# Performance work log

Hardware: AMD Instinct MI355X
Metric: run time of the kernel (lower is better)

The kernel has to match this reference:

```python
import jax, jax.numpy as jnp
import numpy as np

E, K = 8, 2            # num_experts, top_k
H, F = 1024, 1024      # hidden_size, ffn_hidden_size
T = 2048               # tokens (batch*seq)


def setup_inputs() -> dict:
    key = jax.random.key(0)
    k1, k2, k3, k4 = jax.random.split(key, 4)
    x = jax.random.normal(k1, (T, H), jnp.float32)
    gate_w = jax.random.normal(k2, (E, H), jnp.float32) * 0.02   # router FastLinear weight [E, H]
    w1_v1 = jax.random.normal(k3, (E, 2 * F, H), jnp.float32) * 0.02  # cat([w1, v1], dim=0) per expert
    w2 = jax.random.normal(k4, (E, H, F), jnp.float32) * 0.02    # down-proj FastLinear weight [H, F]
    return {"x": x, "gate_w": gate_w, "w1_v1": w1_v1, "w2": w2}


def reference(x, gate_w, w1_v1, w2):
    # Router: logits -> softmax -> top-k gating weights (DBRX style)
    logits = x @ gate_w.T                       # [T, E]
    probs = jax.nn.softmax(logits, axis=-1)
    top_w, top_e = jax.lax.top_k(probs, K)      # [T, K]
    # Dense combine matrix [T, E]: gating weight if expert selected, else 0
    combine = jnp.zeros((x.shape[0], E), x.dtype).at[
        jnp.arange(x.shape[0])[:, None], top_e
    ].add(top_w)
    # Per-expert GLU MLP, batched over experts (grouped GEMM equivalent)
    gv = jnp.einsum('th,efh->etf', x, w1_v1)    # [E, T, 2F]
    g, v = jnp.split(gv, 2, axis=-1)            # each [E, T, F]
    hidden = jax.nn.silu(g) * v                 # [E, T, F]
    outs = jnp.einsum('etf,ehf->eth', hidden, w2)  # [E, T, H]
    # Combine: weighted sum over selected experts
    return jnp.einsum('eth,te->th', outs, combine)  # [T, H]
```

## Files before the change

kernel.cpp:

```cpp
#include <hip/hip_runtime.h>
#include <hip/hip_bf16.h>

#define T_TOK 2048
#define HID   1024
#define FF    1024
#define NE    8
#define CNT_STRIDE 64
#define RTOK 16

using short8   = __attribute__((ext_vector_type(8))) short;
using ushort8v = __attribute__((ext_vector_type(8))) unsigned short;
using f32x4    = __attribute__((ext_vector_type(4))) float;

__device__ __forceinline__ unsigned short f32_to_bf16(float f) {
  union { float f; unsigned int u; } v; v.f = f;
  unsigned int r = v.u + 0x7fffu + ((v.u >> 16) & 1u);
  return (unsigned short)(r >> 16);
}

__global__ __launch_bounds__(256) void convert_kernel(const float* __restrict__ src,
                                                      unsigned short* __restrict__ dst,
                                                      int n4) {
  int i = blockIdx.x * 256 + threadIdx.x;
  if (i >= n4) return;
  const float4 v = ((const float4*)src)[i];
  ushort4 o;
  o.x = f32_to_bf16(v.x); o.y = f32_to_bf16(v.y);
  o.z = f32_to_bf16(v.z); o.w = f32_to_bf16(v.w);
  ((ushort4*)dst)[i] = o;
}

__global__ __launch_bounds__(256) void router_kernel(const float* __restrict__ x,
                                                     const float* __restrict__ gw,
                                                     int* __restrict__ counts,
                                                     int* __restrict__ toks,
                                                     float* __restrict__ wts) {
  __shared__ float gws[NE * HID];
  __shared__ int   s_e[RTOK * 2];
  __shared__ float s_w[RTOK * 2];
  int tid = threadIdx.x;
  int lane = tid & 63, wid = tid >> 6;
  int t0 = blockIdx.x * RTOK;

  float4 greg[8];
#pragma unroll
  for (int j = 0; j < 8; ++j) greg[j] = ((const float4*)gw)[j * 256 + tid];

  float4 xv[4][4];
#pragma unroll
  for (int tk = 0; tk < 4; ++tk) {
    const float4* xr4 = (const float4*)(x + (size_t)(t0 + wid * 4 + tk) * HID);
#pragma unroll
    for (int c = 0; c < 4; ++c) xv[tk][c] = xr4[c * 64 + lane];
  }

#pragma unroll
  for (int j = 0; j < 8; ++j) ((float4*)&gws[0])[j * 256 + tid] = greg[j];
  __syncthreads();

  float acc[4][NE];
#pragma unroll
  for (int tk = 0; tk < 4; ++tk)
#pragma unroll
    for (int e = 0; e < NE; ++e) acc[tk][e] = 0.f;

#pragma unroll
  for (int c = 0; c < 4; ++c) {
#pragma unroll
    for (int e = 0; e < NE; ++e) {
      const float4 gv = *(const float4*)&gws[e * HID + (c * 64 + lane) * 4];
#pragma unroll
      for (int tk = 0; tk < 4; ++tk) {
        acc[tk][e] = fmaf(xv[tk][c].x, gv.x, acc[tk][e]);
        acc[tk][e] = fmaf(xv[tk][c].y, gv.y, acc[tk][e]);
        acc[tk][e] = fmaf(xv[tk][c].z, gv.z, acc[tk][e]);
        acc[tk][e] = fmaf(xv[tk][c].w, gv.w, acc[tk][e]);
      }
    }
  }

#pragma unroll
  for (int tk = 0; tk < 4; ++tk) {
#pragma unroll
    for (int off = 32; off >= 1; off >>= 1) {
#pragma unroll
      for (int e = 0; e < NE; ++e) acc[tk][e] += __shfl_xor(acc[tk][e], off);
    }
    if (lane == 0) {
      int local = wid * 4 + tk;
      float m = acc[tk][0];
#pragma unroll
      for (int e = 1; e < NE; ++e) m = fmaxf(m, acc[tk][e]);
      float p[NE], s = 0.f;
#pragma unroll
      for (int e = 0; e < NE; ++e) { p[e] = __expf(acc[tk][e] - m); s += p[e]; }
      float inv = 1.f / s;

      int e1 = 0; float b1 = p[0];
#pragma unroll
      for (int e = 1; e < NE; ++e) if (p[e] > b1) { b1 = p[e]; e1 = e; }
      int e2 = -1; float b2 = -1.f;
#pragma unroll
      for (int e = 0; e < NE; ++e) if (e != e1 && p[e] > b2) { b2 = p[e]; e2 = e; }

      s_e[local * 2]     = e1;  s_w[local * 2]     = b1 * inv;
      s_e[local * 2 + 1] = e2;  s_w[local * 2 + 1] = b2 * inv;
    }
  }
  __syncthreads();

  if (tid < NE) {
    int c = 0;
#pragma unroll
    for (int i = 0; i < RTOK * 2; ++i) c += (s_e[i] == tid);
    if (c > 0) {
      int base = atomicAdd(&counts[tid * CNT_STRIDE], c);
      int p = 0;
      for (int i = 0; i < RTOK * 2; ++i) {
        if (s_e[i] == tid) {
          toks[tid * T_TOK + base + p] = t0 + (i >> 1);
          wts[tid * T_TOK + base + p] = s_w[i];
          ++p;
        }
      }
    }
  }
}

__global__ __launch_bounds__(256) void gemm1_kernel(const unsigned short* __restrict__ xb,
                                                    const unsigned short* __restrict__ w1b,
                                                    const int* __restrict__ counts,
                                                    const int* __restrict__ toks,
                                                    unsigned short* __restrict__ hidden) {
  int e = blockIdx.z;
  int cnt = counts[e * CNT_STRIDE];
  int m0 = blockIdx.y * 128;
  if (m0 >= cnt) return;
  int n0 = blockIdx.x * 64;
  const unsigned short* W = w1b + (size_t)e * (2 * FF * HID);

  __shared__ unsigned short sA[128 * 64];
  __shared__ unsigned short sBg[64 * 64];
  __shared__ unsigned short sBv[64 * 64];

  int tid = threadIdx.x;
  int lane = tid & 63, wid = tid >> 6;

  const unsigned short* aptr[4]; int adst[4];
#pragma unroll
  for (int j = 0; j < 4; ++j) {
    int q = tid + 256 * j;
    int row = q >> 3, u = q & 7;
    int gr = m0 + row;
    int tok = (gr < cnt) ? toks[e * T_TOK + gr] : 0;
    int su = u ^ (row & 7);
    aptr[j] = xb + (size_t)tok * HID + su * 8;
    adst[j] = row * 64 + u * 8;
  }
  const unsigned short* bgptr[2]; const unsigned short* bvptr[2]; int bdst[2];
#pragma unroll
  for (int j = 0; j < 2; ++j) {
    int q = tid + 256 * j;
    int row = q >> 3, u = q & 7;
    int su = u ^ (row & 7);
    bgptr[j] = W + (size_t)(n0 + row) * HID + su * 8;
    bvptr[j] = W + (size_t)(FF + n0 + row) * HID + su * 8;
    bdst[j] = row * 64 + u * 8;
  }

  f32x4 accg[2][4], accv[2][4];
#pragma unroll
  for (int m = 0; m < 2; ++m)
#pragma unroll
    for (int n = 0; n < 4; ++n) {
      accg[m][n] = (f32x4){0.f, 0.f, 0.f, 0.f};
      accv[m][n] = (f32x4){0.f, 0.f, 0.f, 0.f};
    }

  for (int k0 = 0; k0 < HID; k0 += 64) {
#pragma unroll
    for (int j = 0; j < 4; ++j)
      *(ushort8v*)&sA[adst[j]] = *(const ushort8v*)(aptr[j] + k0);
#pragma unroll
    for (int j = 0; j < 2; ++j) {
      *(ushort8v*)&sBg[bdst[j]] = *(const ushort8v*)(bgptr[j] + k0);
      *(ushort8v*)&sBv[bdst[j]] = *(const ushort8v*)(bvptr[j] + k0);
    }
    __syncthreads();
#pragma unroll
    for (int kk = 0; kk < 2; ++kk) {
      short8 af[2], bgf[4], bvf[4];
#pragma unroll
      for (int m = 0; m < 2; ++m) {
        int row = wid * 32 + m * 16 + (lane & 15);
        int u = (kk * 4 + (lane >> 4)) ^ (row & 7);
        af[m] = *(const short8*)&sA[row * 64 + u * 8];
      }
#pragma unroll
      for (int n = 0; n < 4; ++n) {
        int row = n * 16 + (lane & 15);
        int u = (kk * 4 + (lane >> 4)) ^ (row & 7);
        bgf[n] = *(const short8*)&sBg[row * 64 + u * 8];
        bvf[n] = *(const short8*)&sBv[row * 64 + u * 8];
      }
#pragma unroll
      for (int m = 0; m < 2; ++m)
#pragma unroll
        for (int n = 0; n < 4; ++n) {
          accg[m][n] = __builtin_amdgcn_mfma_f32_16x16x32_bf16(af[m], bgf[n], accg[m][n], 0, 0, 0);
          accv[m][n] = __builtin_amdgcn_mfma_f32_16x16x32_bf16(af[m], bvf[n], accv[m][n], 0, 0, 0);
        }
    }
    __syncthreads();
  }

  unsigned short* Hseg = hidden + (size_t)e * T_TOK * FF;
#pragma unroll
  for (int m = 0; m < 2; ++m) {
#pragma unroll
    for (int j = 0; j < 4; ++j) {
      int row = wid * 32 + m * 16 + (lane >> 4) * 4 + j;
      int gr = m0 + row;
      if (gr < cnt) {
#pragma unroll
        for (int n = 0; n < 4; ++n) {
          int col = n0 + n * 16 + (lane & 15);
          float g = accg[m][n][j];
          float v = accv[m][n][j];
          float val = (g / (1.f + __expf(-g))) * v;
          Hseg[(size_t)gr * FF + col] = f32_to_bf16(val);
        }
      }
    }
  }
}

__global__ __launch_bounds__(256) void gemm2_kernel(const unsigned short* __restrict__ hidden,
                                                    const unsigned short* __restrict__ w2b,
                                                    const int* __restrict__ counts,
                                                    const int* __restrict__ toks,
                                                    const float* __restrict__ wts,
                                                    float* __restrict__ out) {
  int e = blockIdx.z;
  int cnt = counts[e * CNT_STRIDE];
  int m0 = blockIdx.y * 128;
  if (m0 >= cnt) return;
  int n0 = blockIdx.x * 64;
  const unsigned short* A = hidden + (size_t)e * T_TOK * FF;
  const unsigned short* W = w2b + (size_t)e * HID * FF;

  __shared__ unsigned short sA[128 * 64];
  __shared__ unsigned short sB[64 * 64];

  int tid = threadIdx.x;
  int lane = tid & 63, wid = tid >> 6;

  const unsigned short* aptr[4]; int adst[4];
#pragma unroll
  for (int j = 0; j < 4; ++j) {
    int q = tid + 256 * j;
    int row = q >> 3, u = q & 7;
    int su = u ^ (row & 7);
    aptr[j] = A + (size_t)(m0 + row) * FF + su * 8;
    adst[j] = row * 64 + u * 8;
  }
  const unsigned short* bptr[2]; int bdst[2];
#pragma unroll
  for (int j = 0; j < 2; ++j) {
    int q = tid + 256 * j;
    int row = q >> 3, u = q & 7;
    int su = u ^ (row & 7);
    bptr[j] = W + (size_t)(n0 + row) * FF + su * 8;
    bdst[j] = row * 64 + u * 8;
  }

  f32x4 acc[2][4];
#pragma unroll
  for (int m = 0; m < 2; ++m)
#pragma unroll
    for (int n = 0; n < 4; ++n) acc[m][n] = (f32x4){0.f, 0.f, 0.f, 0.f};

  for (int k0 = 0; k0 < FF; k0 += 64) {
#pragma unroll
    for (int j = 0; j < 4; ++j)
      *(ushort8v*)&sA[adst[j]] = *(const ushort8v*)(aptr[j] + k0);
#pragma unroll
    for (int j = 0; j < 2; ++j)
      *(ushort8v*)&sB[bdst[j]] = *(const ushort8v*)(bptr[j] + k0);
    __syncthreads();
#pragma unroll
    for (int kk = 0; kk < 2; ++kk) {
      short8 af[2], bf[4];
#pragma unroll
      for (int m = 0; m < 2; ++m) {
        int row = wid * 32 + m * 16 + (lane & 15);
        int u = (kk * 4 + (lane >> 4)) ^ (row & 7);
        af[m] = *(const short8*)&sA[row * 64 + u * 8];
      }
#pragma unroll
      for (int n = 0; n < 4; ++n) {
        int row = n * 16 + (lane & 15);
        int u = (kk * 4 + (lane >> 4)) ^ (row & 7);
        bf[n] = *(const short8*)&sB[row * 64 + u * 8];
      }
#pragma unroll
      for (int m = 0; m < 2; ++m)
#pragma unroll
        for (int n = 0; n < 4; ++n)
          acc[m][n] = __builtin_amdgcn_mfma_f32_16x16x32_bf16(af[m], bf[n], acc[m][n], 0, 0, 0);
    }
    __syncthreads();
  }

#pragma unroll
  for (int m = 0; m < 2; ++m) {
#pragma unroll
    for (int j = 0; j < 4; ++j) {
      int row = wid * 32 + m * 16 + (lane >> 4) * 4 + j;
      int gr = m0 + row;
      if (gr < cnt) {
        int tok = toks[e * T_TOK + gr];
        float wt = wts[e * T_TOK + gr];
#pragma unroll
        for (int n = 0; n < 4; ++n) {
          int col = n0 + n * 16 + (lane & 15);
          atomicAdd(&out[(size_t)tok * HID + col], acc[m][n][j] * wt);
        }
      }
    }
  }
}

extern "C" void kernel_launch(void* const* d_in, const int* in_sizes, int n_in,
                              void* d_out, int out_size, void* d_ws, size_t ws_size,
                              hipStream_t stream) {
  const float* x  = (const float*)d_in[0];
  const float* gw = (const float*)d_in[1];
  const float* w1 = (const float*)d_in[2];
  const float* w2 = (const float*)d_in[3];
  float* out = (float*)d_out;

  char* ws = (char*)d_ws;
  int*   counts = (int*)ws;
  int*   toks   = (int*)(ws + 4096);
  float* wts    = (float*)(ws + 4096 + 65536);
  unsigned short* xb  = (unsigned short*)(ws + 135168);
  unsigned short* w1b = xb + (size_t)T_TOK * HID;
  unsigned short* w2b = w1b + (size_t)NE * 2 * FF * HID;
  unsigned short* hid = w2b + (size_t)NE * HID * FF;

  hipMemsetAsync(counts, 0, 4096, stream);
  hipMemsetAsync(d_out, 0, (size_t)out_size * sizeof(float), stream);

  convert_kernel<<<(T_TOK * HID / 4 + 255) / 256, 256, 0, stream>>>(x, xb, T_TOK * HID / 4);
  convert_kernel<<<(NE * 2 * FF * HID / 4 + 255) / 256, 256, 0, stream>>>(w1, w1b, NE * 2 * FF * HID / 4);
  convert_kernel<<<(NE * HID * FF / 4 + 255) / 256, 256, 0, stream>>>(w2, w2b, NE * HID * FF / 4);

  router_kernel<<<T_TOK / RTOK, 256, 0, stream>>>(x, gw, counts, toks, wts);

  gemm1_kernel<<<dim3(FF / 64, T_TOK / 128, NE), 256, 0, stream>>>(xb, w1b, counts, toks, hid);
  gemm2_kernel<<<dim3(HID / 64, T_TOK / 128, NE), 256, 0, stream>>>(hid, w2b, counts, toks, wts, out);
}
```

Baseline: 221.4 us.

## Fuse x conversion into router, merge weight converts, use direct global-to-LDS loads

The router now writes the bf16 copy of x while it already holds x in registers, and it processes 8 tokens per block so more blocks launch. The two weight conversions are merged into one launch. Both GEMMs stage tiles with global_load_lds (buffer-to-LDS DMA), which skips the register round-trip. Because the LDS destination must now be linear per lane, the XOR swizzle is kept only on the global source side. This relies on the LDS layout still matching the swizzled reads, and it removes the chance to overlap loads with compute through registers.

```diff
diff --git a/kernel.cpp b/kernel.cpp
--- a/kernel.cpp
+++ b/kernel.cpp
@@ -6,10 +6,9 @@
 #define FF    1024
 #define NE    8
 #define CNT_STRIDE 64
-#define RTOK 16
+#define RBLK 8
 
 using short8   = __attribute__((ext_vector_type(8))) short;
-using ushort8v = __attribute__((ext_vector_type(8))) unsigned short;
 using f32x4    = __attribute__((ext_vector_type(4))) float;
 
 __device__ __forceinline__ unsigned short f32_to_bf16(float f) {
@@ -18,38 +17,50 @@
   return (unsigned short)(r >> 16);
 }
 
-__global__ __launch_bounds__(256) void convert_kernel(const float* __restrict__ src,
-                                                      unsigned short* __restrict__ dst,
-                                                      int n4) {
+__device__ __forceinline__ void gload_lds16(const unsigned short* g, unsigned short* l) {
+  __builtin_amdgcn_global_load_lds(
+      (const __attribute__((address_space(1))) void*)g,
+      (__attribute__((address_space(3))) void*)l, 16, 0, 0);
+}
+
+__global__ __launch_bounds__(256) void convertw_kernel(const float* __restrict__ s1,
+                                                       const float* __restrict__ s2,
+                                                       unsigned short* __restrict__ d1,
+                                                       unsigned short* __restrict__ d2,
+                                                       int n1_4, int ntot_4) {
   int i = blockIdx.x * 256 + threadIdx.x;
-  if (i >= n4) return;
-  const float4 v = ((const float4*)src)[i];
+  if (i >= ntot_4) return;
+  const float* s; unsigned short* d; int k;
+  if (i < n1_4) { s = s1; d = d1; k = i; }
+  else          { s = s2; d = d2; k = i - n1_4; }
+  const float4 v = ((const float4*)s)[k];
   ushort4 o;
   o.x = f32_to_bf16(v.x); o.y = f32_to_bf16(v.y);
   o.z = f32_to_bf16(v.z); o.w = f32_to_bf16(v.w);
-  ((ushort4*)dst)[i] = o;
+  ((ushort4*)d)[k] = o;
 }
 
 __global__ __launch_bounds__(256) void router_kernel(const float* __restrict__ x,
                                                      const float* __restrict__ gw,
                                                      int* __restrict__ counts,
                                                      int* __restrict__ toks,
-                                                     float* __restrict__ wts) {
+                                                     float* __restrict__ wts,
+                                                     unsigned short* __restrict__ xb) {
   __shared__ float gws[NE * HID];
-  __shared__ int   s_e[RTOK * 2];
-  __shared__ float s_w[RTOK * 2];
+  __shared__ int   s_e[RBLK * 2];
+  __shared__ float s_w[RBLK * 2];
   int tid = threadIdx.x;
   int lane = tid & 63, wid = tid >> 6;
-  int t0 = blockIdx.x * RTOK;
+  int t0 = blockIdx.x * RBLK;
 
   float4 greg[8];
 #pragma unroll
   for (int j = 0; j < 8; ++j) greg[j] = ((const float4*)gw)[j * 256 + tid];
 
-  float4 xv[4][4];
-#pragma unroll
-  for (int tk = 0; tk < 4; ++tk) {
-    const float4* xr4 = (const float4*)(x + (size_t)(t0 + wid * 4 + tk) * HID);
+  float4 xv[2][4];
+#pragma unroll
+  for (int tk = 0; tk < 2; ++tk) {
+    const float4* xr4 = (const float4*)(x + (size_t)(t0 + wid * 2 + tk) * HID);
 #pragma unroll
     for (int c = 0; c < 4; ++c) xv[tk][c] = xr4[c * 64 + lane];
   }
@@ -58,9 +69,21 @@
   for (int j = 0; j < 8; ++j) ((float4*)&gws[0])[j * 256 + tid] = greg[j];
   __syncthreads();
 
-  float acc[4][NE];
-#pragma unroll
-  for (int tk = 0; tk < 4; ++tk)
+#pragma unroll
+  for (int tk = 0; tk < 2; ++tk) {
+    unsigned short* xrow = xb + (size_t)(t0 + wid * 2 + tk) * HID;
+#pragma unroll
+    for (int c = 0; c < 4; ++c) {
+      ushort4 o;
+      o.x = f32_to_bf16(xv[tk][c].x); o.y = f32_to_bf16(xv[tk][c].y);
+      o.z = f32_to_bf16(xv[tk][c].z); o.w = f32_to_bf16(xv[tk][c].w);
+      *(ushort4*)&xrow[(c * 64 + lane) * 4] = o;
+    }
+  }
+
+  float acc[2][NE];
+#pragma unroll
+  for (int tk = 0; tk < 2; ++tk)
 #pragma unroll
     for (int e = 0; e < NE; ++e) acc[tk][e] = 0.f;
 
@@ -70,7 +93,7 @@
     for (int e = 0; e < NE; ++e) {
       const float4 gv = *(const float4*)&gws[e * HID + (c * 64 + lane) * 4];
 #pragma unroll
-      for (int tk = 0; tk < 4; ++tk) {
+      for (int tk = 0; tk < 2; ++tk) {
         acc[tk][e] = fmaf(xv[tk][c].x, gv.x, acc[tk][e]);
         acc[tk][e] = fmaf(xv[tk][c].y, gv.y, acc[tk][e]);
         acc[tk][e] = fmaf(xv[tk][c].z, gv.z, acc[tk][e]);
@@ -80,14 +103,14 @@
   }
 
 #pragma unroll
-  for (int tk = 0; tk < 4; ++tk) {
+  for (int tk = 0; tk < 2; ++tk) {
 #pragma unroll
     for (int off = 32; off >= 1; off >>= 1) {
 #pragma unroll
       for (int e = 0; e < NE; ++e) acc[tk][e] += __shfl_xor(acc[tk][e], off);
     }
     if (lane == 0) {
-      int local = wid * 4 + tk;
+      int local = wid * 2 + tk;
       float m = acc[tk][0];
 #pragma unroll
       for (int e = 1; e < NE; ++e) m = fmaxf(m, acc[tk][e]);
@@ -112,11 +135,11 @@
   if (tid < NE) {
     int c = 0;
 #pragma unroll
-    for (int i = 0; i < RTOK * 2; ++i) c += (s_e[i] == tid);
+    for (int i = 0; i < RBLK * 2; ++i) c += (s_e[i] == tid);
     if (c > 0) {
       int base = atomicAdd(&counts[tid * CNT_STRIDE], c);
       int p = 0;
-      for (int i = 0; i < RTOK * 2; ++i) {
+      for (int i = 0; i < RBLK * 2; ++i) {
         if (s_e[i] == tid) {
           toks[tid * T_TOK + base + p] = t0 + (i >> 1);
           wts[tid * T_TOK + base + p] = s_w[i];
@@ -155,7 +178,7 @@
     int tok = (gr < cnt) ? toks[e * T_TOK + gr] : 0;
     int su = u ^ (row & 7);
     aptr[j] = xb + (size_t)tok * HID + su * 8;
-    adst[j] = row * 64 + u * 8;
+    adst[j] = q * 8;
   }
   const unsigned short* bgptr[2]; const unsigned short* bvptr[2]; int bdst[2];
 #pragma unroll
@@ -165,7 +188,7 @@
     int su = u ^ (row & 7);
     bgptr[j] = W + (size_t)(n0 + row) * HID + su * 8;
     bvptr[j] = W + (size_t)(FF + n0 + row) * HID + su * 8;
-    bdst[j] = row * 64 + u * 8;
+    bdst[j] = q * 8;
   }
 
   f32x4 accg[2][4], accv[2][4];
@@ -179,12 +202,11 @@
 
   for (int k0 = 0; k0 < HID; k0 += 64) {
 #pragma unroll
-    for (int j = 0; j < 4; ++j)
-      *(ushort8v*)&sA[adst[j]] = *(const ushort8v*)(aptr[j] + k0);
+    for (int j = 0; j < 4; ++j) gload_lds16(aptr[j] + k0, &sA[adst[j]]);
 #pragma unroll
     for (int j = 0; j < 2; ++j) {
-      *(ushort8v*)&sBg[bdst[j]] = *(const ushort8v*)(bgptr[j] + k0);
-      *(ushort8v*)&sBv[bdst[j]] = *(const ushort8v*)(bvptr[j] + k0);
+      gload_lds16(bgptr[j] + k0, &sBg[bdst[j]]);
+      gload_lds16(bvptr[j] + k0, &sBv[bdst[j]]);
     }
     __syncthreads();
 #pragma unroll
@@ -262,7 +284,7 @@
     int row = q >> 3, u = q & 7;
     int su = u ^ (row & 7);
     aptr[j] = A + (size_t)(m0 + row) * FF + su * 8;
-    adst[j] = row * 64 + u * 8;
+    adst[j] = q * 8;
   }
   const unsigned short* bptr[2]; int bdst[2];
 #pragma unroll
@@ -271,7 +293,7 @@
     int row = q >> 3, u = q & 7;
     int su = u ^ (row & 7);
     bptr[j] = W + (size_t)(n0 + row) * FF + su * 8;
-    bdst[j] = row * 64 + u * 8;
+    bdst[j] = q * 8;
   }
 
   f32x4 acc[2][4];
@@ -282,11 +304,9 @@
 
   for (int k0 = 0; k0 < FF; k0 += 64) {
 #pragma unroll
-    for (int j = 0; j < 4; ++j)
-      *(ushort8v*)&sA[adst[j]] = *(const ushort8v*)(aptr[j] + k0);
-#pragma unroll
-    for (int j = 0; j < 2; ++j)
-      *(ushort8v*)&sB[bdst[j]] = *(const ushort8v*)(bptr[j] + k0);
+    for (int j = 0; j < 4; ++j) gload_lds16(aptr[j] + k0, &sA[adst[j]]);
+#pragma unroll
+    for (int j = 0; j < 2; ++j) gload_lds16(bptr[j] + k0, &sB[bdst[j]]);
     __syncthreads();
 #pragma unroll
     for (int kk = 0; kk < 2; ++kk) {
@@ -352,11 +372,11 @@
   hipMemsetAsync(counts, 0, 4096, stream);
   hipMemsetAsync(d_out, 0, (size_t)out_size * sizeof(float), stream);
 
-  convert_kernel<<<(T_TOK * HID / 4 + 255) / 256, 256, 0, stream>>>(x, xb, T_TOK * HID / 4);
-  convert_kernel<<<(NE * 2 * FF * HID / 4 + 255) / 256, 256, 0, stream>>>(w1, w1b, NE * 2 * FF * HID / 4);
-  convert_kernel<<<(NE * HID * FF / 4 + 255) / 256, 256, 0, stream>>>(w2, w2b, NE * HID * FF / 4);
-
-  router_kernel<<<T_TOK / RTOK, 256, 0, stream>>>(x, gw, counts, toks, wts);
+  router_kernel<<<T_TOK / RBLK, 256, 0, stream>>>(x, gw, counts, toks, wts, xb);
+
+  const int n1_4 = NE * 2 * FF * HID / 4;
+  const int ntot_4 = n1_4 + NE * HID * FF / 4;
+  convertw_kernel<<<(ntot_4 + 255) / 256, 256, 0, stream>>>(w1, w2, w1b, w2b, n1_4, ntot_4);
 
   gemm1_kernel<<<dim3(FF / 64, T_TOK / 128, NE), 256, 0, stream>>>(xb, w1b, counts, toks, hid);
   gemm2_kernel<<<dim3(HID / 64, T_TOK / 128, NE), 256, 0, stream>>>(hid, w2b, counts, toks, wts, out);
```

Result: faster. 207.9 us (-6.1%).
